# Optimization experiments

Hardware: AMD Instinct MI355X
Metric: run time of the kernel (lower is better)

Reference implementation:

```python
import jax, jax.numpy as jnp
import numpy as np

B, Q, D = 8, 1, 4096
NH, NKV, HD = 32, 8, 128
KV = 4096
ROPE_BASE = 10000.0


def setup_inputs() -> dict:
    key = jax.random.key(0)
    ks = jax.random.split(key, 10)
    s = 0.02  # realistic init scale for weights
    return {
        "hidden_states": jax.random.normal(ks[0], (B, Q, D), jnp.float32),
        "past_k": jax.random.normal(ks[1], (B, NH, KV, HD), jnp.float32),
        "past_v": jax.random.normal(ks[2], (B, NH, KV, HD), jnp.float32),
        "Wq": jax.random.normal(ks[3], (NH * HD, D), jnp.float32) * s,
        "bq": jax.random.normal(ks[4], (NH * HD,), jnp.float32) * s,
        "Wk": jax.random.normal(ks[5], (NKV * HD, D), jnp.float32) * s,
        "bk": jax.random.normal(ks[6], (NKV * HD,), jnp.float32) * s,
        "Wv": jax.random.normal(ks[7], (NKV * HD, D), jnp.float32) * s,
        "bv": jax.random.normal(ks[8], (NKV * HD,), jnp.float32) * s,
        "Wo": jax.random.normal(ks[9], (D, NH * HD), jnp.float32) * s,
        "position_ids": KV,  # current decode position (past length)
    }


def _rope(x, pos0):
    # x: [B, H, Q, HD]; rotate_half-style RoPE at positions pos0..pos0+Q-1
    half = HD // 2
    inv_freq = 1.0 / (ROPE_BASE ** (jnp.arange(half, dtype=jnp.float32) / half))
    pos = (pos0 + jnp.arange(Q)).astype(jnp.float32)          # [Q]
    ang = pos[:, None] * inv_freq[None, :]                    # [Q, half]
    cos = jnp.concatenate([jnp.cos(ang), jnp.cos(ang)], -1)   # [Q, HD]
    sin = jnp.concatenate([jnp.sin(ang), jnp.sin(ang)], -1)
    x1, x2 = x[..., :half], x[..., half:]
    rot = jnp.concatenate([-x2, x1], axis=-1)
    return x * cos + rot * sin


def reference(hidden_states, past_k, past_v, Wq, bq, Wk, bk, Wv, bv, Wo, position_ids):
    # QKV projections (Qwen: biased q/k/v, unbiased o)
    q = hidden_states @ Wq.T + bq   # [B, Q, NH*HD]
    k = hidden_states @ Wk.T + bk   # [B, Q, NKV*HD]
    v = hidden_states @ Wv.T + bv
    q = q.reshape(B, Q, NH, HD).transpose(0, 2, 1, 3)    # [B, NH, Q, HD]
    k = k.reshape(B, Q, NKV, HD).transpose(0, 2, 1, 3)   # [B, NKV, Q, HD]
    v = v.reshape(B, Q, NKV, HD).transpose(0, 2, 1, 3)
    # RoPE on current tokens only (past cache already rotated)
    q = _rope(q, position_ids)
    k = _rope(k, position_ids)
    # GQA repeat_interleave to full head count
    rep = NH // NKV
    k = jnp.repeat(k, rep, axis=1)   # [B, NH, Q, HD]
    v = jnp.repeat(v, rep, axis=1)
    # Assemble streaming KV window: past cache is stored post-repeat
    k = jnp.concatenate([past_k, k], axis=2)   # [B, NH, KV+Q, HD]
    v = jnp.concatenate([past_v, v], axis=2)
    scale = jnp.float32(1.0 / np.sqrt(HD))
    scores = jnp.einsum("bhqd,bhkd->bhqk", q, k) * scale   # [B, NH, Q, KV+Q]
    # causal: query positions KV..KV+Q-1 attend to key positions <= own pos
    qpos = KV + jnp.arange(Q)
    kpos = jnp.arange(KV + Q)
    mask = qpos[:, None] >= kpos[None, :]
    scores = jnp.where(mask, scores, jnp.float32(-1e30))
    attn = jax.nn.softmax(scores, axis=-1)
    ctx = jnp.einsum("bhqk,bhkd->bhqd", attn, v)           # [B, NH, Q, HD]
    ctx = ctx.transpose(0, 2, 1, 3).reshape(B, Q, NH * HD)
    return ctx @ Wo.T   # [B, Q, D]
```

## Files before the change

### kernel.cpp

```cpp
#include <hip/hip_runtime.h>
#include <hip/hip_bf16.h>
#include <math.h>

#define BB 8
#define DD 4096
#define NHQ 32
#define NKV 8
#define HD 128
#define KVL 4096
#define NSPLIT 32
#define CHUNK (KVL / NSPLIT)
#define SCALE 0.08838834764831845f

#define OFF_QROPE 0
#define OFF_KROPE (OFF_QROPE + BB*NHQ*HD)
#define OFF_VRAW  (OFF_KROPE + BB*NKV*HD)
#define OFF_PART  (OFF_VRAW  + BB*NKV*HD)
#define PART_STRIDE 132
#define OFF_CTX   (OFF_PART + BB*NHQ*NSPLIT*PART_STRIDE)

typedef float f32x4 __attribute__((ext_vector_type(4)));

__device__ __forceinline__ float4 ntload4(const float4* p) {
    f32x4 v = __builtin_nontemporal_load((const f32x4*)p);
    return make_float4(v.x, v.y, v.z, v.w);
}

__device__ __forceinline__ float dot4(const float4 a, const float4 b) {
    return fmaf(a.x, b.x, fmaf(a.y, b.y, fmaf(a.z, b.z, a.w*b.w)));
}

__global__ __launch_bounds__(256) void k_qkv(
    const float* __restrict__ hs,
    const float* __restrict__ Wq, const float* __restrict__ bq,
    const float* __restrict__ Wk, const float* __restrict__ bk,
    const float* __restrict__ Wv, const float* __restrict__ bv,
    const int* __restrict__ posp,
    float* __restrict__ ws)
{
    const int wid  = threadIdx.x >> 6;
    const int lane = threadIdx.x & 63;
    const int w    = blockIdx.x * 4 + wid;

    const float* W; const float* bias; float* dst; int dstride; int r1; int i; bool rope;
    if (w < 2048) {
        const int h = w >> 6; i = w & 63; r1 = h*HD + i;
        W = Wq; bias = bq; dst = ws + OFF_QROPE; dstride = NHQ*HD; rope = true;
    } else if (w < 2560) {
        const int w2 = w - 2048; const int h = w2 >> 6; i = w2 & 63; r1 = h*HD + i;
        W = Wk; bias = bk; dst = ws + OFF_KROPE; dstride = NKV*HD; rope = true;
    } else {
        const int w3 = w - 2560; const int h = w3 >> 6; i = w3 & 63; r1 = h*HD + i;
        W = Wv; bias = bv; dst = ws + OFF_VRAW; dstride = NKV*HD; rope = false;
    }
    const int r2 = r1 + 64;

    const double pos = (double)posp[0];
    const double ang = pos * pow(10000.0, -(double)i / 64.0);
    const float c = (float)cos(ang), s = (float)sin(ang);

    const float4* WrA = (const float4*)(W + (size_t)r1 * DD);
    const float4* WrB = (const float4*)(W + (size_t)r2 * DD);
    const float4* H   = (const float4*)hs;

    float accA[BB], accB[BB];
    #pragma unroll
    for (int b = 0; b < BB; ++b) { accA[b] = 0.f; accB[b] = 0.f; }

    for (int it = 0; it < DD/256; ++it) {
        const int idx = it*64 + lane;
        const float4 wa = ntload4(&WrA[idx]);
        const float4 wb = ntload4(&WrB[idx]);
        #pragma unroll
        for (int b = 0; b < BB; ++b) {
            const float4 h4 = H[b*(DD/4) + idx];
            accA[b] = fmaf(wa.x, h4.x, fmaf(wa.y, h4.y, fmaf(wa.z, h4.z, fmaf(wa.w, h4.w, accA[b]))));
            accB[b] = fmaf(wb.x, h4.x, fmaf(wb.y, h4.y, fmaf(wb.z, h4.z, fmaf(wb.w, h4.w, accB[b]))));
        }
    }
    #pragma unroll
    for (int b = 0; b < BB; ++b) {
        float va = accA[b], vb = accB[b];
        #pragma unroll
        for (int off = 32; off; off >>= 1) {
            va += __shfl_xor(va, off, 64);
            vb += __shfl_xor(vb, off, 64);
        }
        accA[b] = va; accB[b] = vb;
    }
    if (lane == 0) {
        const float b1 = bias[r1], b2 = bias[r2];
        #pragma unroll
        for (int b = 0; b < BB; ++b) {
            const float a1 = accA[b] + b1;
            const float a2 = accB[b] + b2;
            float o1, o2;
            if (rope) { o1 = fmaf(a1, c, -a2*s); o2 = fmaf(a2, c, a1*s); }
            else      { o1 = a1;                 o2 = a2; }
            dst[(size_t)b*dstride + r1] = o1;
            dst[(size_t)b*dstride + r2] = o2;
        }
    }
}

__global__ __launch_bounds__(256) void k_attn(
    const float* __restrict__ Kc, const float* __restrict__ Vc,
    float* __restrict__ ws)
{
    __shared__ float sc_lds[4][CHUNK];

    const int wid  = threadIdx.x >> 6;
    const int lane = threadIdx.x & 63;
    const int sub  = lane >> 5, l32 = lane & 31;
    const int task  = blockIdx.x * 4 + wid;
    const int pair  = task >> 5;
    const int split = task & (NSPLIT - 1);
    const int b = pair >> 5, h = pair & 31;
    float* swv = sc_lds[wid];

    const float4 q4 = ((const float4*)(ws + OFF_QROPE + (size_t)pair * HD))[l32];
    const size_t base = ((size_t)pair * KVL + (size_t)split * CHUNK) * HD;
    const float4* Kp = (const float4*)(Kc + base);
    const float4* Vp = (const float4*)(Vc + base);

    float m0 = -1e30f;
    for (int it = 0; it < CHUNK/8; ++it) {
        const int r0 = it*8 + sub;
        const float4 k0 = ntload4(&Kp[(r0+0)*32 + l32]);
        const float4 k1 = ntload4(&Kp[(r0+2)*32 + l32]);
        const float4 k2 = ntload4(&Kp[(r0+4)*32 + l32]);
        const float4 k3 = ntload4(&Kp[(r0+6)*32 + l32]);
        float s0 = dot4(q4, k0), s1 = dot4(q4, k1);
        float s2 = dot4(q4, k2), s3 = dot4(q4, k3);
        #pragma unroll
        for (int off = 16; off; off >>= 1) {
            s0 += __shfl_xor(s0, off, 64);
            s1 += __shfl_xor(s1, off, 64);
            s2 += __shfl_xor(s2, off, 64);
            s3 += __shfl_xor(s3, off, 64);
        }
        s0 *= SCALE; s1 *= SCALE; s2 *= SCALE; s3 *= SCALE;
        m0 = fmaxf(m0, fmaxf(fmaxf(s0, s1), fmaxf(s2, s3)));
        if (l32 == 0) {
            swv[r0+0] = s0; swv[r0+2] = s1; swv[r0+4] = s2; swv[r0+6] = s3;
        }
    }
    float m = fmaxf(m0, __shfl_xor(m0, 32, 64));

    float l = 0.f;
    float4 acc = {0.f, 0.f, 0.f, 0.f};
    for (int it = 0; it < CHUNK/8; ++it) {
        const int r0 = it*8 + sub;
        const float4 v0 = ntload4(&Vp[(r0+0)*32 + l32]);
        const float4 v1 = ntload4(&Vp[(r0+2)*32 + l32]);
        const float4 v2 = ntload4(&Vp[(r0+4)*32 + l32]);
        const float4 v3 = ntload4(&Vp[(r0+6)*32 + l32]);
        const float e0 = __expf(swv[r0+0] - m);
        const float e1 = __expf(swv[r0+2] - m);
        const float e2 = __expf(swv[r0+4] - m);
        const float e3 = __expf(swv[r0+6] - m);
        l += (e0 + e1) + (e2 + e3);
        acc.x += fmaf(e0, v0.x, e1*v1.x) + fmaf(e2, v2.x, e3*v3.x);
        acc.y += fmaf(e0, v0.y, e1*v1.y) + fmaf(e2, v2.y, e3*v3.y);
        acc.z += fmaf(e0, v0.z, e1*v1.z) + fmaf(e2, v2.z, e3*v3.z);
        acc.w += fmaf(e0, v0.w, e1*v1.w) + fmaf(e2, v2.w, e3*v3.w);
    }

    if (split == NSPLIT - 1 && sub == 0) {
        const float4 kn = ((const float4*)(ws + OFF_KROPE + (size_t)(b*NKV + (h>>2)) * HD))[l32];
        const float4 vn = ((const float4*)(ws + OFF_VRAW  + (size_t)(b*NKV + (h>>2)) * HD))[l32];
        float sv = dot4(q4, kn);
        #pragma unroll
        for (int off = 16; off; off >>= 1) sv += __shfl_xor(sv, off, 64);
        sv *= SCALE;
        const float newm = fmaxf(m, sv);
        const float r_ = __expf(m - newm);
        const float e  = __expf(sv - newm);
        m = newm;
        l = fmaf(l, r_, e);
        acc.x = fmaf(acc.x, r_, e*vn.x);
        acc.y = fmaf(acc.y, r_, e*vn.y);
        acc.z = fmaf(acc.z, r_, e*vn.z);
        acc.w = fmaf(acc.w, r_, e*vn.w);
    }

    const float M  = fmaxf(m, __shfl_xor(m, 32, 64));
    const float r2_ = __expf(m - M);
    l *= r2_; acc.x *= r2_; acc.y *= r2_; acc.z *= r2_; acc.w *= r2_;
    l     += __shfl_xor(l,     32, 64);
    acc.x += __shfl_xor(acc.x, 32, 64);
    acc.y += __shfl_xor(acc.y, 32, 64);
    acc.z += __shfl_xor(acc.z, 32, 64);
    acc.w += __shfl_xor(acc.w, 32, 64);

    if (sub == 0) {
        float* pp = ws + OFF_PART + ((size_t)pair * NSPLIT + split) * PART_STRIDE;
        ((float4*)pp)[l32] = acc;
        if (l32 == 0) { pp[HD] = M; pp[HD+1] = l; }
    }
}

__global__ __launch_bounds__(128) void k_combine(float* __restrict__ ws)
{
    const int pair = blockIdx.x;
    const int d = threadIdx.x;
    const float* pp = ws + OFF_PART + (size_t)pair * NSPLIT * PART_STRIDE;
    __shared__ float sm[NSPLIT], sl[NSPLIT];
    if (d < NSPLIT) { sm[d] = pp[d*PART_STRIDE + HD]; sl[d] = pp[d*PART_STRIDE + HD + 1]; }
    __syncthreads();
    float M = -1e30f;
    #pragma unroll
    for (int s = 0; s < NSPLIT; ++s) M = fmaxf(M, sm[s]);
    float L = 0.f, acc = 0.f;
    #pragma unroll 8
    for (int s = 0; s < NSPLIT; ++s) {
        const float w = expf(sm[s] - M);
        L += sl[s] * w;
        acc = fmaf(pp[s*PART_STRIDE + d], w, acc);
    }
    ws[OFF_CTX + (size_t)pair*HD + d] = acc / L;
}

__global__ __launch_bounds__(256) void k_oproj(
    const float* __restrict__ Wo, const float* __restrict__ ws, float* __restrict__ out)
{
    const int wid  = threadIdx.x >> 6;
    const int lane = threadIdx.x & 63;
    const int row  = blockIdx.x * 4 + wid;
    const float4* Wr = (const float4*)(Wo + (size_t)row * DD);
    const float4* C  = (const float4*)(ws + OFF_CTX);
    float acc[BB];
    #pragma unroll
    for (int b = 0; b < BB; ++b) acc[b] = 0.f;
    for (int it = 0; it < DD/256; ++it) {
        const int idx = it*64 + lane;
        const float4 w4 = ntload4(&Wr[idx]);
        #pragma unroll
        for (int b = 0; b < BB; ++b) {
            const float4 h4 = C[b*(DD/4) + idx];
            acc[b] = fmaf(w4.x, h4.x, fmaf(w4.y, h4.y, fmaf(w4.z, h4.z, fmaf(w4.w, h4.w, acc[b]))));
        }
    }
    #pragma unroll
    for (int b = 0; b < BB; ++b) {
        float v = acc[b];
        #pragma unroll
        for (int off = 32; off; off >>= 1) v += __shfl_xor(v, off, 64);
        if (lane == 0) out[(size_t)b*DD + row] = v;
    }
}

extern "C" void kernel_launch(void* const* d_in, const int* in_sizes, int n_in,
                              void* d_out, int out_size, void* d_ws, size_t ws_size,
                              hipStream_t stream)
{
    const float* hs  = (const float*)d_in[0];
    const float* pk  = (const float*)d_in[1];
    const float* pv  = (const float*)d_in[2];
    const float* Wq  = (const float*)d_in[3];
    const float* bq  = (const float*)d_in[4];
    const float* Wk  = (const float*)d_in[5];
    const float* bk  = (const float*)d_in[6];
    const float* Wv  = (const float*)d_in[7];
    const float* bv  = (const float*)d_in[8];
    const float* Wo  = (const float*)d_in[9];
    const int*   pos = (const int*)d_in[10];
    float* out = (float*)d_out;
    float* ws  = (float*)d_ws;

    k_qkv    <<<3072/4,          256, 0, stream>>>(hs, Wq, bq, Wk, bk, Wv, bv, pos, ws);
    k_attn   <<<BB*NHQ*NSPLIT/4, 256, 0, stream>>>(pk, pv, ws);
    k_combine<<<BB*NHQ,          128, 0, stream>>>(ws);
    k_oproj  <<<4096/4,          256, 0, stream>>>(Wo, ws, out);
}
```

Baseline: 246.0 us.

## Split attention into separate score and value-accumulate kernels via workspace

The fused split-KV attention kernel becomes two kernels. The first streams K, computes scaled scores, folds in the new token, and writes exponentiated scores plus the per-split max and sum to workspace. The second streams V, reads those weights into LDS and accumulates the context. The aim is a simpler, leaner inner loop for each stream, at the cost of an extra launch, a kernel boundary that stops K and V reads overlapping, and extra workspace traffic for the scores.

```diff
diff --git a/kernel.cpp b/kernel.cpp
--- a/kernel.cpp
+++ b/kernel.cpp
@@ -15,7 +15,9 @@
 #define OFF_QROPE 0
 #define OFF_KROPE (OFF_QROPE + BB*NHQ*HD)
 #define OFF_VRAW  (OFF_KROPE + BB*NKV*HD)
-#define OFF_PART  (OFF_VRAW  + BB*NKV*HD)
+#define OFF_SC    (OFF_VRAW + BB*NKV*HD)
+#define SC_STRIDE 132
+#define OFF_PART  (OFF_SC + BB*NHQ*NSPLIT*SC_STRIDE)
 #define PART_STRIDE 132
 #define OFF_CTX   (OFF_PART + BB*NHQ*NSPLIT*PART_STRIDE)
 
@@ -103,9 +105,8 @@
     }
 }
 
-__global__ __launch_bounds__(256) void k_attn(
-    const float* __restrict__ Kc, const float* __restrict__ Vc,
-    float* __restrict__ ws)
+__global__ __launch_bounds__(256) void k_score(
+    const float* __restrict__ Kc, float* __restrict__ ws)
 {
     __shared__ float sc_lds[4][CHUNK];
 
@@ -119,9 +120,7 @@
     float* swv = sc_lds[wid];
 
     const float4 q4 = ((const float4*)(ws + OFF_QROPE + (size_t)pair * HD))[l32];
-    const size_t base = ((size_t)pair * KVL + (size_t)split * CHUNK) * HD;
-    const float4* Kp = (const float4*)(Kc + base);
-    const float4* Vp = (const float4*)(Vc + base);
+    const float4* Kp = (const float4*)(Kc + ((size_t)pair * KVL + (size_t)split * CHUNK) * HD);
 
     float m0 = -1e30f;
     for (int it = 0; it < CHUNK/8; ++it) {
@@ -147,7 +146,53 @@
     }
     float m = fmaxf(m0, __shfl_xor(m0, 32, 64));
 
-    float l = 0.f;
+    const bool last = (split == NSPLIT - 1);
+    float e_new = 0.f;
+    if (last) {
+        const float4 kn = ((const float4*)(ws + OFF_KROPE + (size_t)(b*NKV + (h>>2)) * HD))[l32];
+        float sv = dot4(q4, kn);
+        #pragma unroll
+        for (int off = 16; off; off >>= 1) sv += __shfl_xor(sv, off, 64);
+        sv *= SCALE;
+        m = fmaxf(m, sv);
+        e_new = __expf(sv - m);
+    }
+
+    float* sc = ws + OFF_SC + ((size_t)pair * NSPLIT + split) * SC_STRIDE;
+    const float ea = __expf(swv[lane]      - m);
+    const float eb = __expf(swv[lane + 64] - m);
+    sc[lane]      = ea;
+    sc[lane + 64] = eb;
+    float ls = ea + eb;
+    #pragma unroll
+    for (int off = 32; off; off >>= 1) ls += __shfl_xor(ls, off, 64);
+    if (lane == 0) {
+        if (last) sc[128] = e_new;
+        sc[129] = m;
+        sc[130] = ls + e_new;
+    }
+}
+
+__global__ __launch_bounds__(256) void k_vacc(
+    const float* __restrict__ Vc, float* __restrict__ ws)
+{
+    __shared__ float e_lds[4][CHUNK];
+
+    const int wid  = threadIdx.x >> 6;
+    const int lane = threadIdx.x & 63;
+    const int sub  = lane >> 5, l32 = lane & 31;
+    const int task  = blockIdx.x * 4 + wid;
+    const int pair  = task >> 5;
+    const int split = task & (NSPLIT - 1);
+    const int b = pair >> 5, h = pair & 31;
+    float* ev = e_lds[wid];
+
+    const float* sc = ws + OFF_SC + ((size_t)pair * NSPLIT + split) * SC_STRIDE;
+    ev[lane]      = sc[lane];
+    ev[lane + 64] = sc[lane + 64];
+
+    const float4* Vp = (const float4*)(Vc + ((size_t)pair * KVL + (size_t)split * CHUNK) * HD);
+
     float4 acc = {0.f, 0.f, 0.f, 0.f};
     for (int it = 0; it < CHUNK/8; ++it) {
         const int r0 = it*8 + sub;
@@ -155,11 +200,10 @@
         const float4 v1 = ntload4(&Vp[(r0+2)*32 + l32]);
         const float4 v2 = ntload4(&Vp[(r0+4)*32 + l32]);
         const float4 v3 = ntload4(&Vp[(r0+6)*32 + l32]);
-        const float e0 = __expf(swv[r0+0] - m);
-        const float e1 = __expf(swv[r0+2] - m);
-        const float e2 = __expf(swv[r0+4] - m);
-        const float e3 = __expf(swv[r0+6] - m);
-        l += (e0 + e1) + (e2 + e3);
+        const float e0 = ev[r0+0];
+        const float e1 = ev[r0+2];
+        const float e2 = ev[r0+4];
+        const float e3 = ev[r0+6];
         acc.x += fmaf(e0, v0.x, e1*v1.x) + fmaf(e2, v2.x, e3*v3.x);
         acc.y += fmaf(e0, v0.y, e1*v1.y) + fmaf(e2, v2.y, e3*v3.y);
         acc.z += fmaf(e0, v0.z, e1*v1.z) + fmaf(e2, v2.z, e3*v3.z);
@@ -167,27 +211,14 @@
     }
 
     if (split == NSPLIT - 1 && sub == 0) {
-        const float4 kn = ((const float4*)(ws + OFF_KROPE + (size_t)(b*NKV + (h>>2)) * HD))[l32];
-        const float4 vn = ((const float4*)(ws + OFF_VRAW  + (size_t)(b*NKV + (h>>2)) * HD))[l32];
-        float sv = dot4(q4, kn);
-        #pragma unroll
-        for (int off = 16; off; off >>= 1) sv += __shfl_xor(sv, off, 64);
-        sv *= SCALE;
-        const float newm = fmaxf(m, sv);
-        const float r_ = __expf(m - newm);
-        const float e  = __expf(sv - newm);
-        m = newm;
-        l = fmaf(l, r_, e);
-        acc.x = fmaf(acc.x, r_, e*vn.x);
-        acc.y = fmaf(acc.y, r_, e*vn.y);
-        acc.z = fmaf(acc.z, r_, e*vn.z);
-        acc.w = fmaf(acc.w, r_, e*vn.w);
-    }
-
-    const float M  = fmaxf(m, __shfl_xor(m, 32, 64));
-    const float r2_ = __expf(m - M);
-    l *= r2_; acc.x *= r2_; acc.y *= r2_; acc.z *= r2_; acc.w *= r2_;
-    l     += __shfl_xor(l,     32, 64);
+        const float4 vn = ((const float4*)(ws + OFF_VRAW + (size_t)(b*NKV + (h>>2)) * HD))[l32];
+        const float en = sc[128];
+        acc.x = fmaf(en, vn.x, acc.x);
+        acc.y = fmaf(en, vn.y, acc.y);
+        acc.z = fmaf(en, vn.z, acc.z);
+        acc.w = fmaf(en, vn.w, acc.w);
+    }
+
     acc.x += __shfl_xor(acc.x, 32, 64);
     acc.y += __shfl_xor(acc.y, 32, 64);
     acc.z += __shfl_xor(acc.z, 32, 64);
@@ -196,7 +227,6 @@
     if (sub == 0) {
         float* pp = ws + OFF_PART + ((size_t)pair * NSPLIT + split) * PART_STRIDE;
         ((float4*)pp)[l32] = acc;
-        if (l32 == 0) { pp[HD] = M; pp[HD+1] = l; }
     }
 }
 
@@ -204,9 +234,10 @@
 {
     const int pair = blockIdx.x;
     const int d = threadIdx.x;
-    const float* pp = ws + OFF_PART + (size_t)pair * NSPLIT * PART_STRIDE;
+    const float* scb = ws + OFF_SC   + (size_t)pair * NSPLIT * SC_STRIDE;
+    const float* pp  = ws + OFF_PART + (size_t)pair * NSPLIT * PART_STRIDE;
     __shared__ float sm[NSPLIT], sl[NSPLIT];
-    if (d < NSPLIT) { sm[d] = pp[d*PART_STRIDE + HD]; sl[d] = pp[d*PART_STRIDE + HD + 1]; }
+    if (d < NSPLIT) { sm[d] = scb[d*SC_STRIDE + 129]; sl[d] = scb[d*SC_STRIDE + 130]; }
     __syncthreads();
     float M = -1e30f;
     #pragma unroll
@@ -269,7 +300,8 @@
     float* ws  = (float*)d_ws;
 
     k_qkv    <<<3072/4,          256, 0, stream>>>(hs, Wq, bq, Wk, bk, Wv, bv, pos, ws);
-    k_attn   <<<BB*NHQ*NSPLIT/4, 256, 0, stream>>>(pk, pv, ws);
+    k_score  <<<BB*NHQ*NSPLIT/4, 256, 0, stream>>>(pk, ws);
+    k_vacc   <<<BB*NHQ*NSPLIT/4, 256, 0, stream>>>(pv, ws);
     k_combine<<<BB*NHQ,          128, 0, stream>>>(ws);
     k_oproj  <<<4096/4,          256, 0, stream>>>(Wo, ws, out);
 }
```

Result: slower. 254.1 us (+3.3%).
